# Kernel optimization log

Hardware: AMD Instinct MI355X
Metric: run time of the kernel (lower is better)

## Reference

```python
import jax, jax.numpy as jnp
import numpy as np

L_LAYERS, D, H, V, S, B = 12, 1024, 16, 50257, 512, 4
DH = D // H
DFF = 4 * D
EPS = 1e-6
STD = 0.02


def setup_inputs() -> dict:
    key = jax.random.key(0)
    ks = jax.random.split(key, 16)
    n = lambda k, shp: (jax.random.normal(k, shp, dtype=jnp.float32) * STD)
    inp = {
        'in_idx': jax.random.randint(ks[0], (B, S), 0, V, dtype=jnp.int32),
        'tok_emb': n(ks[1], (V, D)),          # tied with out_head
        'pos_emb': n(ks[2], (S, D)),
        # per-layer stacked params; Linear stored as [in, out] so y = x @ W
        'Wq': n(ks[3], (L_LAYERS, D, D)),
        'Wk': n(ks[4], (L_LAYERS, D, D)),
        'Wv': n(ks[5], (L_LAYERS, D, D)),
        'Wo': n(ks[6], (L_LAYERS, D, D)),
        'bo': jnp.zeros((L_LAYERS, D), jnp.float32),
        'W1': n(ks[7], (L_LAYERS, D, DFF)),
        'b1': jnp.zeros((L_LAYERS, DFF), jnp.float32),
        'W2': n(ks[8], (L_LAYERS, DFF, D)),
        'b2': jnp.zeros((L_LAYERS, D), jnp.float32),
        'ln1_s': jnp.ones((L_LAYERS, D), jnp.float32),
        'ln1_b': jnp.zeros((L_LAYERS, D), jnp.float32),
        'ln2_s': jnp.ones((L_LAYERS, D), jnp.float32),
        'ln2_b': jnp.zeros((L_LAYERS, D), jnp.float32),
        'lnf_s': jnp.ones((D,), jnp.float32),
        'lnf_b': jnp.zeros((D,), jnp.float32),
    }
    return inp


def _layernorm(x, scale, shift):
    mean = jnp.mean(x, axis=-1, keepdims=True)
    var = jnp.mean(jnp.square(x - mean), axis=-1, keepdims=True)  # unbiased=False
    return scale * (x - mean) / jnp.sqrt(var + EPS) + shift


def _gelu(x):
    c = jnp.sqrt(jnp.asarray(2.0 / jnp.pi, x.dtype))
    return 0.5 * x * (1.0 + jnp.tanh(c * (x + 0.044715 * x * x * x)))


def _gpt_forward(in_idx, tok_emb, pos_emb, Wq, Wk, Wv, Wo, bo, W1, b1, W2, b2,
                 ln1_s, ln1_b, ln2_s, ln2_b, lnf_s, lnf_b):
    b, s = in_idx.shape
    x = tok_emb[in_idx] + pos_emb[:s]  # [B,S,D]
    causal = jnp.triu(jnp.ones((s, s), bool), k=1)  # True above diagonal
    scale = 1.0 / jnp.sqrt(jnp.asarray(DH, x.dtype))
    for i in range(L_LAYERS):
        # --- attention sublayer ---
        h = _layernorm(x, ln1_s[i], ln1_b[i])
        q = (h @ Wq[i]).reshape(b, s, H, DH)
        k = (h @ Wk[i]).reshape(b, s, H, DH)
        v = (h @ Wv[i]).reshape(b, s, H, DH)
        scores = jnp.einsum('bqhd,bkhd->bhqk', q, k)
        scores = jnp.where(causal, -jnp.inf, scores) * scale
        attn = jax.nn.softmax(scores, axis=-1)
        ctx = jnp.einsum('bhqk,bkhd->bqhd', attn, v).reshape(b, s, D)
        x = x + ctx @ Wo[i] + bo[i]
        # --- feed-forward sublayer ---
        h = _layernorm(x, ln2_s[i], ln2_b[i])
        x = x + _gelu(h @ W1[i] + b1[i]) @ W2[i] + b2[i]
    x = _layernorm(x, lnf_s, lnf_b)
    logits = x @ tok_emb.T  # tied out head (no bias)
    return logits


def reference(in_idx, tok_emb, pos_emb, Wq, Wk, Wv, Wo, bo, W1, b1, W2, b2,
              ln1_s, ln1_b, ln2_s, ln2_b, lnf_s, lnf_b):
    return _gpt_forward(in_idx, tok_emb, pos_emb, Wq, Wk, Wv, Wo, bo, W1, b1,
                        W2, b2, ln1_s, ln1_b, ln2_s, ln2_b, lnf_s, lnf_b)
```

## Files before the change

### kernel.cpp

```cpp
#include <hip/hip_runtime.h>


#define LL 12
#define DM 1024
#define NH 16
#define DHD 64
#define NV 50257
#define NVP 50432
#define SQ 512
#define NB 4
#define DF 4096
#define MR (NB * SQ)

typedef short bf16x8 __attribute__((ext_vector_type(8)));
typedef float f32x4 __attribute__((ext_vector_type(4)));
typedef unsigned short u16;

__device__ __forceinline__ u16 f2b(float f) {
  unsigned u = __float_as_uint(f);
  u += 0x7fff + ((u >> 16) & 1);
  return (u16)(u >> 16);
}

__device__ __forceinline__ void gload16(const u16* g, u16* l) {
  __builtin_amdgcn_global_load_lds(
      (const __attribute__((address_space(1))) unsigned*)g,
      (__attribute__((address_space(3))) unsigned*)l, 16, 0, 0);
}

template <int MODE, int TBM, int TBN, int MTLOG>
__global__ __launch_bounds__(256, 2) void gemm_k(
    const u16* __restrict__ A, const u16* __restrict__ B, void* __restrict__ Cp,
    void* __restrict__ Cp2, void* __restrict__ Cp3,
    const float* __restrict__ bias, int N, int K, int lda, int ldb, int ldc) {
  int id = blockIdx.x;
  int q8 = gridDim.x >> 3;
  int swz = (id & 7) * q8 + (id >> 3);
  int mt = swz & ((1 << MTLOG) - 1), nt = swz >> MTLOG;
  int m0 = mt * TBM, n0 = nt * TBN;

  __shared__ u16 As[2][TBM * 64];
  __shared__ u16 Bs[2][TBN * 64];

  int t = threadIdx.x, lane = t & 63, wave = t >> 6;
  int wm = wave >> 1, wn = wave & 1;
  int lr = lane & 15, g = lane >> 4;
  int srow = lane >> 3;
  int sxcol = ((lane & 7) ^ (lane >> 3)) << 3;
  int rsw = (lr & 7) << 3;
  constexpr int FM = TBM / 32, FN = TBN / 32;
  constexpr int CA = TBM / 32, CB = TBN / 32;

  f32x4 acc[FM][FN];
#pragma unroll
  for (int i = 0; i < FM; ++i)
#pragma unroll
    for (int j = 0; j < FN; ++j) acc[i][j] = (f32x4){0.f, 0.f, 0.f, 0.f};

  auto stage = [&](int buf, int kt) {
    int k0 = kt * 64;
#pragma unroll
    for (int v = 0; v < CA; ++v) {
      int c = v * 4 + wave;
      gload16(A + (size_t)(m0 + c * 8 + srow) * lda + k0 + sxcol,
              &As[buf][c * 512]);
    }
#pragma unroll
    for (int v = 0; v < CB; ++v) {
      int c = v * 4 + wave;
      gload16(B + (size_t)(n0 + c * 8 + srow) * ldb + k0 + sxcol,
              &Bs[buf][c * 512]);
    }
  };

  auto compute = [&](int buf) {
    bf16x8 af[FM][2], bq[FN][2];
#pragma unroll
    for (int ks = 0; ks < 2; ++ks) {
      int co = (ks * 32 + g * 8) ^ rsw;
#pragma unroll
      for (int i = 0; i < FM; ++i)
        af[i][ks] =
            *(const bf16x8*)&As[buf][(wm * (TBM / 2) + i * 16 + lr) * 64 + co];
#pragma unroll
      for (int j = 0; j < FN; ++j)
        bq[j][ks] =
            *(const bf16x8*)&Bs[buf][(wn * (TBN / 2) + j * 16 + lr) * 64 + co];
    }
#pragma unroll
    for (int ks = 0; ks < 2; ++ks)
#pragma unroll
      for (int i = 0; i < FM; ++i)
#pragma unroll
        for (int j = 0; j < FN; ++j)
          acc[i][j] = __builtin_amdgcn_mfma_f32_16x16x32_bf16(
              af[i][ks], bq[j][ks], acc[i][j], 0, 0, 0);
  };

  int nk = K >> 6;
  stage(0, 0);
  __syncthreads();
  int cur = 0;
  for (int kt = 0; kt < nk - 1; ++kt) {
    stage(cur ^ 1, kt + 1);
    compute(cur);
    __syncthreads();
    cur ^= 1;
  }
  compute(cur);

  int rb = g * 4;
#pragma unroll
  for (int i = 0; i < FM; ++i) {
#pragma unroll
    for (int j = 0; j < FN; ++j) {
      int m = m0 + wm * (TBM / 2) + i * 16 + rb;
      int n = n0 + wn * (TBN / 2) + j * 16 + lr;
      f32x4 a = acc[i][j];
      if constexpr (MODE == 1) {
        float* C = (float*)Cp;
        float bv = bias[n];
#pragma unroll
        for (int r = 0; r < 4; ++r) {
          size_t ix = (size_t)(m + r) * ldc + n;
          C[ix] += a[r] + bv;
        }
      } else if constexpr (MODE == 2) {
        u16* C = (u16*)Cp;
        float bv = bias[n];
#pragma unroll
        for (int r = 0; r < 4; ++r) {
          float u2 = a[r] + bv;
          float gl =
              0.5f * u2 *
              (1.f + tanhf(0.7978845608f * (u2 + 0.044715f * u2 * u2 * u2)));
          C[(size_t)(m + r) * ldc + n] = f2b(gl);
        }
      } else if constexpr (MODE == 7) {
        int sel = n >> 10, nn = n & 1023;
        if (sel < 2) {
          u16* C = sel == 0 ? (u16*)Cp : (u16*)Cp2;
#pragma unroll
          for (int r = 0; r < 4; ++r) C[(size_t)(m + r) * ldc + nn] = f2b(a[r]);
        } else {
          u16* C = (u16*)Cp3;
          int bb = m >> 9, s2 = m & (SQ - 1);
          ushort4 w4;
          w4.x = f2b(a[0]); w4.y = f2b(a[1]);
          w4.z = f2b(a[2]); w4.w = f2b(a[3]);
          *(ushort4*)&C[((size_t)bb * DM + nn) * SQ + s2] = w4;
        }
      }
    }
  }
}

__global__ __launch_bounds__(512, 1) void gemmL_k(const u16* __restrict__ A,
                                                  const u16* __restrict__ B,
                                                  float* __restrict__ C) {
  int id = blockIdx.x;
  int q8 = gridDim.x >> 3;
  int swz = (id & 7) * q8 + (id >> 3);
  int mt = swz & 7, nt = swz >> 3;
  int m0 = mt * 256, n0 = nt * 256;

  __shared__ u16 As[2][256 * 64];
  __shared__ u16 Bs[3][256 * 64];

  int t = threadIdx.x, lane = t & 63, wave = t >> 6;
  int wm = wave >> 2, wn = wave & 3;
  int lr = lane & 15, g = lane >> 4;
  int rsw = (lr & 7) << 3;

  f32x4 acc[8][4];
#pragma unroll
  for (int i = 0; i < 8; ++i)
#pragma unroll
    for (int j = 0; j < 4; ++j) acc[i][j] = (f32x4){0.f, 0.f, 0.f, 0.f};

  auto stageA = [&](int slot, int kt) {
    int k0 = kt * 64;
#pragma unroll
    for (int v = 0; v < 4; ++v) {
      int c = v * 512 + t;
      int row = c >> 3, cc = c & 7;
      gload16(A + (size_t)(m0 + row) * DM + k0 + ((cc ^ (row & 7)) << 3),
              &As[slot][c * 8]);
    }
  };
  auto stageB = [&](int slot, int kt) {
    int k0 = kt * 64;
#pragma unroll
    for (int v = 0; v < 4; ++v) {
      int c = v * 512 + t;
      int row = c >> 3, cc = c & 7;
      gload16(B + (size_t)(n0 + row) * DM + k0 + ((cc ^ (row & 7)) << 3),
              &Bs[slot][c * 8]);
    }
  };
  auto compute = [&](int sa, int sb) {
#pragma unroll
    for (int ks = 0; ks < 2; ++ks) {
      int co = (ks * 32 + g * 8) ^ rsw;
      bf16x8 af[8], bq[4];
#pragma unroll
      for (int i = 0; i < 8; ++i)
        af[i] = *(const bf16x8*)&As[sa][(wm * 128 + i * 16 + lr) * 64 + co];
#pragma unroll
      for (int j = 0; j < 4; ++j)
        bq[j] = *(const bf16x8*)&Bs[sb][(wn * 64 + j * 16 + lr) * 64 + co];
      __builtin_amdgcn_s_setprio(1);
#pragma unroll
      for (int i = 0; i < 8; ++i)
#pragma unroll
        for (int j = 0; j < 4; ++j)
          acc[i][j] = __builtin_amdgcn_mfma_f32_16x16x32_bf16(
              af[i], bq[j], acc[i][j], 0, 0, 0);
      __builtin_amdgcn_s_setprio(0);
    }
  };

  stageB(0, 0); stageA(0, 0); stageB(1, 1); stageA(1, 1); stageB(2, 2);
  int sb = 0;
#pragma unroll 1
  for (int kt = 0; kt < 14; ++kt) {
    asm volatile("s_waitcnt vmcnt(12)" ::: "memory");
    __builtin_amdgcn_s_barrier();
    __builtin_amdgcn_sched_barrier(0);
    compute(kt & 1, sb);
    __builtin_amdgcn_s_barrier();
    __builtin_amdgcn_sched_barrier(0);
    stageA(kt & 1, kt + 2);
    if (kt < 13) stageB(sb, kt + 3);
    sb = sb + 1 == 3 ? 0 : sb + 1;
  }
  asm volatile("s_waitcnt vmcnt(8)" ::: "memory");
  __builtin_amdgcn_s_barrier();
  __builtin_amdgcn_sched_barrier(0);
  compute(0, 2);
  __builtin_amdgcn_s_barrier();
  __builtin_amdgcn_sched_barrier(0);
  asm volatile("s_waitcnt vmcnt(0)" ::: "memory");
  __builtin_amdgcn_s_barrier();
  __builtin_amdgcn_sched_barrier(0);
  compute(1, 0);

  int rb = g * 4;
#pragma unroll
  for (int i = 0; i < 8; ++i) {
#pragma unroll
    for (int j = 0; j < 4; ++j) {
      int m = m0 + wm * 128 + i * 16 + rb;
      int n = n0 + wn * 64 + j * 16 + lr;
      if (n < NV) {
        f32x4 a = acc[i][j];
#pragma unroll
        for (int r = 0; r < 4; ++r) C[(size_t)(m + r) * NV + n] = a[r];
      }
    }
  }
}

__global__ __launch_bounds__(256) void fattn_k(const u16* __restrict__ qb,
                                               const u16* __restrict__ kb,
                                               const u16* __restrict__ vt,
                                               u16* __restrict__ cx) {
  int id = blockIdx.x;
  int qt = id >> 6, bh = id & 63;
  int b = bh >> 4, hh = bh & 15;
  int t = threadIdx.x, lane = t & 63, w = t >> 6;
  int lr = lane & 15, g = lane >> 4;

  __shared__ u16 Kt[64 * 72];
  __shared__ u16 Vt[64 * 72];
  __shared__ u16 Pl[4 * 16 * 72];

  int qw = qt * 64 + w * 16;

  bf16x8 aQ[2];
#pragma unroll
  for (int f = 0; f < 2; ++f)
    aQ[f] = *(const bf16x8*)&qb[(size_t)(b * SQ + qw + lr) * DM + hh * DHD +
                                f * 32 + g * 8];

  f32x4 o[4];
#pragma unroll
  for (int j = 0; j < 4; ++j) o[j] = (f32x4){0.f, 0.f, 0.f, 0.f};
  f32x4 m4 = (f32x4){-3e38f, -3e38f, -3e38f, -3e38f};
  f32x4 l4 = (f32x4){0.f, 0.f, 0.f, 0.f};
  u16* Pw = &Pl[w * 16 * 72];

  for (int kt = 0; kt <= qt; ++kt) {
    int k0 = kt * 64;
#pragma unroll
    for (int it = 0; it < 2; ++it) {
      int c = t + it * 256;
      int row = c >> 3, ch = c & 7;
      int4 kv = *(const int4*)&kb[(size_t)(b * SQ + k0 + row) * DM + hh * DHD +
                                  ch * 8];
      int4 vv = *(const int4*)&vt[(size_t)(b * DM + hh * DHD + row) * SQ + k0 +
                                  ch * 8];
      *(int4*)&Kt[row * 72 + ch * 8] = kv;
      *(int4*)&Vt[row * 72 + ch * 8] = vv;
    }
    __syncthreads();

    f32x4 s[4];
#pragma unroll
    for (int j = 0; j < 4; ++j) s[j] = (f32x4){0.f, 0.f, 0.f, 0.f};
#pragma unroll
    for (int j = 0; j < 4; ++j)
#pragma unroll
      for (int f = 0; f < 2; ++f) {
        bf16x8 bk = *(const bf16x8*)&Kt[(j * 16 + lr) * 72 + f * 32 + g * 8];
        s[j] =
            __builtin_amdgcn_mfma_f32_16x16x32_bf16(aQ[f], bk, s[j], 0, 0, 0);
      }
#pragma unroll
    for (int j = 0; j < 4; ++j) {
      int kcol = k0 + j * 16 + lr;
#pragma unroll
      for (int r = 0; r < 4; ++r) {
        float sv = s[j][r] * 0.125f;
        if (kt == qt && kcol > qw + g * 4 + r) sv = -1e30f;
        s[j][r] = sv;
      }
    }
    f32x4 fr;
#pragma unroll
    for (int r = 0; r < 4; ++r) {
      float v = fmaxf(fmaxf(s[0][r], s[1][r]), fmaxf(s[2][r], s[3][r]));
#pragma unroll
      for (int d = 1; d < 16; d <<= 1) v = fmaxf(v, __shfl_xor(v, d));
      float mn = fmaxf(m4[r], v);
      fr[r] = __expf(m4[r] - mn);
      m4[r] = mn;
    }
#pragma unroll
    for (int j = 0; j < 4; ++j)
#pragma unroll
      for (int r = 0; r < 4; ++r) o[j][r] *= fr[r];
    f32x4 ps = (f32x4){0.f, 0.f, 0.f, 0.f};
#pragma unroll
    for (int j = 0; j < 4; ++j)
#pragma unroll
      for (int r = 0; r < 4; ++r) {
        float p = __expf(s[j][r] - m4[r]);
        s[j][r] = p;
        ps[r] += p;
      }
#pragma unroll
    for (int r = 0; r < 4; ++r) {
      float v = ps[r];
#pragma unroll
      for (int d = 1; d < 16; d <<= 1) v += __shfl_xor(v, d);
      l4[r] = l4[r] * fr[r] + v;
    }
#pragma unroll
    for (int j = 0; j < 4; ++j)
#pragma unroll
      for (int r = 0; r < 4; ++r)
        Pw[(g * 4 + r) * 72 + j * 16 + lr] = f2b(s[j][r]);
#pragma unroll
    for (int f = 0; f < 2; ++f) {
      bf16x8 ap = *(const bf16x8*)&Pw[lr * 72 + f * 32 + g * 8];
#pragma unroll
      for (int j = 0; j < 4; ++j) {
        bf16x8 bv = *(const bf16x8*)&Vt[(j * 16 + lr) * 72 + f * 32 + g * 8];
        o[j] = __builtin_amdgcn_mfma_f32_16x16x32_bf16(ap, bv, o[j], 0, 0, 0);
      }
    }
    __syncthreads();
  }

#pragma unroll
  for (int r = 0; r < 4; ++r) {
    float inv = 1.f / l4[r];
#pragma unroll
    for (int j = 0; j < 4; ++j)
      cx[(size_t)(b * SQ + qw + g * 4 + r) * DM + hh * DHD + j * 16 + lr] =
          f2b(o[j][r] * inv);
  }
}

__global__ __launch_bounds__(256) void transpln_k(
    const float* __restrict__ Wq, const float* __restrict__ Wk,
    const float* __restrict__ Wv, const float* __restrict__ Wo,
    const float* __restrict__ W1, const float* __restrict__ W2,
    u16* __restrict__ wb, const float* __restrict__ x,
    const float* __restrict__ sc, const float* __restrict__ sh,
    u16* __restrict__ o) {
  __shared__ u16 tl[64][72];
  __shared__ float red[8];
  int t = threadIdx.x;
  if (blockIdx.x < 3072) {
    int id = blockIdx.x;
    const float* src;
    u16* dst;
    int K, N, ktile, ntile;
    if (id < 1024) {
      int mat = id >> 8, rem = id & 255;
      ntile = rem & 15; ktile = rem >> 4;
      src = mat == 0 ? Wq : mat == 1 ? Wk : mat == 2 ? Wv : Wo;
      dst = wb + (size_t)mat * DM * DM;
      K = DM; N = DM;
    } else if (id < 2048) {
      int rem = id - 1024;
      ntile = rem & 63; ktile = rem >> 6;
      src = W1; dst = wb + (size_t)4 * DM * DM;
      K = DM; N = DF;
    } else {
      int rem = id - 2048;
      ntile = rem & 15; ktile = rem >> 4;
      src = W2; dst = wb + (size_t)4 * DM * DM + (size_t)DM * DF;
      K = DF; N = DM;
    }
    int n0 = ntile * 64, k0 = ktile * 64;
    int tn = (t & 15) * 4, tk = t >> 4;
#pragma unroll
    for (int it = 0; it < 4; ++it) {
      int k = tk + it * 16;
      float4 v = *(const float4*)(src + (size_t)(k0 + k) * N + n0 + tn);
      tl[tn + 0][k] = f2b(v.x);
      tl[tn + 1][k] = f2b(v.y);
      tl[tn + 2][k] = f2b(v.z);
      tl[tn + 3][k] = f2b(v.w);
    }
    __syncthreads();
    int wn = t >> 3, wk = (t & 7) * 8;
#pragma unroll
    for (int it = 0; it < 2; ++it) {
      int n = wn + it * 32;
      int4 v = *(const int4*)&tl[n][wk];
      *(int4*)(dst + (size_t)(n0 + n) * K + k0 + wk) = v;
    }
  } else {
    int row = blockIdx.x - 3072;
    const float* xr = x + (size_t)row * DM;
    float4 v = *(const float4*)(xr + t * 4);
    float s = v.x + v.y + v.z + v.w;
#pragma unroll
    for (int d = 32; d; d >>= 1) s += __shfl_xor(s, d);
    if ((t & 63) == 0) red[t >> 6] = s;
    __syncthreads();
    float mean = (red[0] + red[1] + red[2] + red[3]) * (1.f / DM);
    float dx = v.x - mean, dy = v.y - mean, dz = v.z - mean, dw = v.w - mean;
    float s2 = dx * dx + dy * dy + dz * dz + dw * dw;
#pragma unroll
    for (int d = 32; d; d >>= 1) s2 += __shfl_xor(s2, d);
    if ((t & 63) == 0) red[4 + (t >> 6)] = s2;
    __syncthreads();
    float var = (red[4] + red[5] + red[6] + red[7]) * (1.f / DM);
    float rstd = 1.f / sqrtf(var + 1e-6f);
    float4 gg = *(const float4*)(sc + t * 4);
    float4 b = *(const float4*)(sh + t * 4);
    ushort4 w4;
    w4.x = f2b(gg.x * (dx * rstd) + b.x);
    w4.y = f2b(gg.y * (dy * rstd) + b.y);
    w4.z = f2b(gg.z * (dz * rstd) + b.z);
    w4.w = f2b(gg.w * (dw * rstd) + b.w);
    *(ushort4*)(o + (size_t)row * DM + t * 4) = w4;
  }
}

__global__ __launch_bounds__(256) void ln_k(const float* __restrict__ x,
                                            const float* __restrict__ sc,
                                            const float* __restrict__ sh,
                                            u16* __restrict__ o) {
  int row = blockIdx.x, t = threadIdx.x;
  const float* xr = x + (size_t)row * DM;
  float4 v = *(const float4*)(xr + t * 4);
  float s = v.x + v.y + v.z + v.w;
#pragma unroll
  for (int d = 32; d; d >>= 1) s += __shfl_xor(s, d);
  __shared__ float red[8];
  if ((t & 63) == 0) red[t >> 6] = s;
  __syncthreads();
  float mean = (red[0] + red[1] + red[2] + red[3]) * (1.f / DM);
  float dx = v.x - mean, dy = v.y - mean, dz = v.z - mean, dw = v.w - mean;
  float s2 = dx * dx + dy * dy + dz * dz + dw * dw;
#pragma unroll
  for (int d = 32; d; d >>= 1) s2 += __shfl_xor(s2, d);
  if ((t & 63) == 0) red[4 + (t >> 6)] = s2;
  __syncthreads();
  float var = (red[4] + red[5] + red[6] + red[7]) * (1.f / DM);
  float rstd = 1.f / sqrtf(var + 1e-6f);
  float4 g = *(const float4*)(sc + t * 4);
  float4 b = *(const float4*)(sh + t * 4);
  ushort4 w4;
  w4.x = f2b(g.x * (dx * rstd) + b.x);
  w4.y = f2b(g.y * (dy * rstd) + b.y);
  w4.z = f2b(g.z * (dz * rstd) + b.z);
  w4.w = f2b(g.w * (dw * rstd) + b.w);
  *(ushort4*)(o + (size_t)row * DM + t * 4) = w4;
}

__global__ __launch_bounds__(256) void embtok_k(const int* __restrict__ idx,
                                                const float* __restrict__ tok,
                                                const float* __restrict__ pos,
                                                float* __restrict__ x,
                                                u16* __restrict__ tokT) {
  int t = threadIdx.x;
  if (blockIdx.x < MR) {
    int row = blockIdx.x;
    int s = row & (SQ - 1);
    int id = idx[row];
    float4 a = *(const float4*)(tok + (size_t)id * DM + t * 4);
    float4 p = *(const float4*)(pos + (size_t)s * DM + t * 4);
    a.x += p.x; a.y += p.y; a.z += p.z; a.w += p.w;
    *(float4*)(x + (size_t)row * DM + t * 4) = a;
  } else {
    size_t r = blockIdx.x - MR;
    ushort4 w = {0, 0, 0, 0};
    if (r < NV) {
      float4 v = *(const float4*)(tok + r * DM + t * 4);
      w.x = f2b(v.x); w.y = f2b(v.y); w.z = f2b(v.z); w.w = f2b(v.w);
    }
    *(ushort4*)(tokT + r * DM + t * 4) = w;
  }
}

extern "C" void kernel_launch(void* const* d_in, const int* in_sizes, int n_in,
                              void* d_out, int out_size, void* d_ws,
                              size_t ws_size, hipStream_t stream) {
  const int* idx = (const int*)d_in[0];
  const float* tok = (const float*)d_in[1];
  const float* pos = (const float*)d_in[2];
  const float* Wq = (const float*)d_in[3];
  const float* Wk = (const float*)d_in[4];
  const float* Wv = (const float*)d_in[5];
  const float* Wo = (const float*)d_in[6];
  const float* bo = (const float*)d_in[7];
  const float* W1 = (const float*)d_in[8];
  const float* b1 = (const float*)d_in[9];
  const float* W2 = (const float*)d_in[10];
  const float* b2 = (const float*)d_in[11];
  const float* ln1s = (const float*)d_in[12];
  const float* ln1b = (const float*)d_in[13];
  const float* ln2s = (const float*)d_in[14];
  const float* ln2b = (const float*)d_in[15];
  const float* lnfs = (const float*)d_in[16];
  const float* lnfb = (const float*)d_in[17];
  float* out = (float*)d_out;

  char* w = (char*)d_ws;
  float* x = (float*)w;  w += (size_t)MR * DM * 4;
  u16* h = (u16*)w;      w += (size_t)MR * DM * 2;
  u16* qb = (u16*)w;     w += (size_t)MR * DM * 2;
  u16* kb = (u16*)w;     w += (size_t)MR * DM * 2;
  u16* vt = (u16*)w;     w += (size_t)NB * DM * SQ * 2;
  u16* ff = (u16*)w;     w += (size_t)MR * DF * 2;
  u16* wb = (u16*)w;     w += ((size_t)4 * DM * DM + 2 * (size_t)DM * DF) * 2;
  u16* tokT = (u16*)w;
  u16* cx = h;
  u16* wo_b = wb + (size_t)3 * DM * DM;
  u16* wb1 = wb + (size_t)4 * DM * DM;
  u16* wb2 = wb1 + (size_t)DM * DF;

  dim3 T(256);
  embtok_k<<<MR + NVP, T, 0, stream>>>(idx, tok, pos, x, tokT);
  for (int l = 0; l < LL; ++l) {
    size_t wo_ = (size_t)l * DM * DM;
    size_t w1_ = (size_t)l * DM * DF;
    transpln_k<<<5120, T, 0, stream>>>(Wq + wo_, Wk + wo_, Wv + wo_, Wo + wo_,
                                       W1 + w1_, W2 + w1_, wb, x, ln1s + l * DM,
                                       ln1b + l * DM, h);
    gemm_k<7, 64, 128, 5><<<768, T, 0, stream>>>(
        h, wb, qb, kb, vt, nullptr, 3 * DM, DM, DM, DM, DM);
    fattn_k<<<512, T, 0, stream>>>(qb, kb, vt, cx);
    gemm_k<1, 64, 64, 5><<<512, T, 0, stream>>>(
        cx, wo_b, x, nullptr, nullptr, bo + l * DM, DM, DM, DM, DM, DM);
    ln_k<<<MR, T, 0, stream>>>(x, ln2s + l * DM, ln2b + l * DM, h);
    gemm_k<2, 128, 128, 4><<<512, T, 0, stream>>>(
        h, wb1, ff, nullptr, nullptr, b1 + l * DF, DF, DM, DM, DM, DF);
    gemm_k<1, 64, 64, 5><<<512, T, 0, stream>>>(
        ff, wb2, x, nullptr, nullptr, b2 + l * DM, DM, DF, DF, DF, DM);
  }
  ln_k<<<MR, T, 0, stream>>>(x, lnfs, lnfb, h);
  gemmL_k<<<1576, dim3(512), 0, stream>>>(h, tokT, out);
}
```

Measured before the change: 2.248 ms.

## Fuse weight fp32-to-bf16 transpose into GEMM B-tile loading

Removes the per-layer transpose/convert kernel and instead has each GEMM load fp32 weights directly from global memory into registers, convert to bf16, and write them transposed into a padded LDS tile. The QKV GEMM selects among Wq/Wk/Wv by column block. This avoids writing and re-reading the bf16 weight copy each layer, but every GEMM block now reads fp32 weights (twice the bytes) redundantly across M tiles and does conversion work plus non-async LDS scatter stores with a padded stride.

```diff
diff --git a/kernel.cpp b/kernel.cpp
--- a/kernel.cpp
+++ b/kernel.cpp
@@ -28,10 +28,13 @@
       (__attribute__((address_space(3))) unsigned*)l, 16, 0, 0);
 }
 
+#define BPAD 70
+
 template <int MODE, int TBM, int TBN, int MTLOG>
 __global__ __launch_bounds__(256, 2) void gemm_k(
-    const u16* __restrict__ A, const u16* __restrict__ B, void* __restrict__ Cp,
-    void* __restrict__ Cp2, void* __restrict__ Cp3,
+    const u16* __restrict__ A, const void* __restrict__ Bp,
+    const void* __restrict__ Bp2, const void* __restrict__ Bp3,
+    void* __restrict__ Cp, void* __restrict__ Cp2, void* __restrict__ Cp3,
     const float* __restrict__ bias, int N, int K, int lda, int ldb, int ldc) {
   int id = blockIdx.x;
   int q8 = gridDim.x >> 3;
@@ -39,8 +42,19 @@
   int mt = swz & ((1 << MTLOG) - 1), nt = swz >> MTLOG;
   int m0 = mt * TBM, n0 = nt * TBN;
 
+  const float* Bf;
+  int bn0 = n0;
+  if constexpr (MODE == 7) {
+    int sel0 = n0 >> 10;
+    Bf = sel0 == 0 ? (const float*)Bp
+                   : sel0 == 1 ? (const float*)Bp2 : (const float*)Bp3;
+    bn0 = n0 & 1023;
+  } else {
+    Bf = (const float*)Bp;
+  }
+
   __shared__ u16 As[2][TBM * 64];
-  __shared__ u16 Bs[2][TBN * 64];
+  __shared__ u16 Bs[2][TBN * BPAD];
 
   int t = threadIdx.x, lane = t & 63, wave = t >> 6;
   int wm = wave >> 1, wn = wave & 1;
@@ -49,7 +63,10 @@
   int sxcol = ((lane & 7) ^ (lane >> 3)) << 3;
   int rsw = (lr & 7) << 3;
   constexpr int FM = TBM / 32, FN = TBN / 32;
-  constexpr int CA = TBM / 32, CB = TBN / 32;
+  constexpr int CA = TBM / 32;
+
+  constexpr int LN_ = TBN / 4, KS = 256 / LN_, BP = TBN / 16;
+  int tk = t / LN_, tn = (t % LN_) * 4;
 
   f32x4 acc[FM][FN];
 #pragma unroll
@@ -57,7 +74,25 @@
 #pragma unroll
     for (int j = 0; j < FN; ++j) acc[i][j] = (f32x4){0.f, 0.f, 0.f, 0.f};
 
-  auto stage = [&](int buf, int kt) {
+  float4 breg[BP];
+  auto loadB = [&](int kt) {
+    int k0 = kt * 64;
+#pragma unroll
+    for (int p = 0; p < BP; ++p)
+      breg[p] =
+          *(const float4*)(Bf + (size_t)(k0 + p * KS + tk) * ldb + bn0 + tn);
+  };
+  auto writeB = [&](int buf) {
+#pragma unroll
+    for (int p = 0; p < BP; ++p) {
+      u16* d = &Bs[buf][tn * BPAD + p * KS + tk];
+      d[0] = f2b(breg[p].x);
+      d[BPAD] = f2b(breg[p].y);
+      d[2 * BPAD] = f2b(breg[p].z);
+      d[3 * BPAD] = f2b(breg[p].w);
+    }
+  };
+  auto stageA = [&](int buf, int kt) {
     int k0 = kt * 64;
 #pragma unroll
     for (int v = 0; v < CA; ++v) {
@@ -65,27 +100,21 @@
       gload16(A + (size_t)(m0 + c * 8 + srow) * lda + k0 + sxcol,
               &As[buf][c * 512]);
     }
-#pragma unroll
-    for (int v = 0; v < CB; ++v) {
-      int c = v * 4 + wave;
-      gload16(B + (size_t)(n0 + c * 8 + srow) * ldb + k0 + sxcol,
-              &Bs[buf][c * 512]);
-    }
-  };
-
+  };
   auto compute = [&](int buf) {
     bf16x8 af[FM][2], bq[FN][2];
 #pragma unroll
     for (int ks = 0; ks < 2; ++ks) {
       int co = (ks * 32 + g * 8) ^ rsw;
+      int cb = ks * 32 + g * 8;
 #pragma unroll
       for (int i = 0; i < FM; ++i)
         af[i][ks] =
             *(const bf16x8*)&As[buf][(wm * (TBM / 2) + i * 16 + lr) * 64 + co];
 #pragma unroll
       for (int j = 0; j < FN; ++j)
-        bq[j][ks] =
-            *(const bf16x8*)&Bs[buf][(wn * (TBN / 2) + j * 16 + lr) * 64 + co];
+        bq[j][ks] = *(const bf16x8*)&Bs[buf][(wn * (TBN / 2) + j * 16 + lr) *
+                                                 BPAD + cb];
     }
 #pragma unroll
     for (int ks = 0; ks < 2; ++ks)
@@ -98,12 +127,16 @@
   };
 
   int nk = K >> 6;
-  stage(0, 0);
+  loadB(0);
+  stageA(0, 0);
+  writeB(0);
   __syncthreads();
   int cur = 0;
   for (int kt = 0; kt < nk - 1; ++kt) {
-    stage(cur ^ 1, kt + 1);
+    loadB(kt + 1);
+    stageA(cur ^ 1, kt + 1);
     compute(cur);
+    writeB(cur ^ 1);
     __syncthreads();
     cur ^= 1;
   }
@@ -380,86 +413,6 @@
     for (int j = 0; j < 4; ++j)
       cx[(size_t)(b * SQ + qw + g * 4 + r) * DM + hh * DHD + j * 16 + lr] =
           f2b(o[j][r] * inv);
-  }
-}
-
-__global__ __launch_bounds__(256) void transpln_k(
-    const float* __restrict__ Wq, const float* __restrict__ Wk,
-    const float* __restrict__ Wv, const float* __restrict__ Wo,
-    const float* __restrict__ W1, const float* __restrict__ W2,
-    u16* __restrict__ wb, const float* __restrict__ x,
-    const float* __restrict__ sc, const float* __restrict__ sh,
-    u16* __restrict__ o) {
-  __shared__ u16 tl[64][72];
-  __shared__ float red[8];
-  int t = threadIdx.x;
-  if (blockIdx.x < 3072) {
-    int id = blockIdx.x;
-    const float* src;
-    u16* dst;
-    int K, N, ktile, ntile;
-    if (id < 1024) {
-      int mat = id >> 8, rem = id & 255;
-      ntile = rem & 15; ktile = rem >> 4;
-      src = mat == 0 ? Wq : mat == 1 ? Wk : mat == 2 ? Wv : Wo;
-      dst = wb + (size_t)mat * DM * DM;
-      K = DM; N = DM;
-    } else if (id < 2048) {
-      int rem = id - 1024;
-      ntile = rem & 63; ktile = rem >> 6;
-      src = W1; dst = wb + (size_t)4 * DM * DM;
-      K = DM; N = DF;
-    } else {
-      int rem = id - 2048;
-      ntile = rem & 15; ktile = rem >> 4;
-      src = W2; dst = wb + (size_t)4 * DM * DM + (size_t)DM * DF;
-      K = DF; N = DM;
-    }
-    int n0 = ntile * 64, k0 = ktile * 64;
-    int tn = (t & 15) * 4, tk = t >> 4;
-#pragma unroll
-    for (int it = 0; it < 4; ++it) {
-      int k = tk + it * 16;
-      float4 v = *(const float4*)(src + (size_t)(k0 + k) * N + n0 + tn);
-      tl[tn + 0][k] = f2b(v.x);
-      tl[tn + 1][k] = f2b(v.y);
-      tl[tn + 2][k] = f2b(v.z);
-      tl[tn + 3][k] = f2b(v.w);
-    }
-    __syncthreads();
-    int wn = t >> 3, wk = (t & 7) * 8;
-#pragma unroll
-    for (int it = 0; it < 2; ++it) {
-      int n = wn + it * 32;
-      int4 v = *(const int4*)&tl[n][wk];
-      *(int4*)(dst + (size_t)(n0 + n) * K + k0 + wk) = v;
-    }
-  } else {
-    int row = blockIdx.x - 3072;
-    const float* xr = x + (size_t)row * DM;
-    float4 v = *(const float4*)(xr + t * 4);
-    float s = v.x + v.y + v.z + v.w;
-#pragma unroll
-    for (int d = 32; d; d >>= 1) s += __shfl_xor(s, d);
-    if ((t & 63) == 0) red[t >> 6] = s;
-    __syncthreads();
-    float mean = (red[0] + red[1] + red[2] + red[3]) * (1.f / DM);
-    float dx = v.x - mean, dy = v.y - mean, dz = v.z - mean, dw = v.w - mean;
-    float s2 = dx * dx + dy * dy + dz * dz + dw * dw;
-#pragma unroll
-    for (int d = 32; d; d >>= 1) s2 += __shfl_xor(s2, d);
-    if ((t & 63) == 0) red[4 + (t >> 6)] = s2;
-    __syncthreads();
-    float var = (red[4] + red[5] + red[6] + red[7]) * (1.f / DM);
-    float rstd = 1.f / sqrtf(var + 1e-6f);
-    float4 gg = *(const float4*)(sc + t * 4);
-    float4 b = *(const float4*)(sh + t * 4);
-    ushort4 w4;
-    w4.x = f2b(gg.x * (dx * rstd) + b.x);
-    w4.y = f2b(gg.y * (dy * rstd) + b.y);
-    w4.z = f2b(gg.z * (dz * rstd) + b.z);
-    w4.w = f2b(gg.w * (dw * rstd) + b.w);
-    *(ushort4*)(o + (size_t)row * DM + t * 4) = w4;
   }
 }
 
@@ -550,31 +503,29 @@
   u16* kb = (u16*)w;     w += (size_t)MR * DM * 2;
   u16* vt = (u16*)w;     w += (size_t)NB * DM * SQ * 2;
   u16* ff = (u16*)w;     w += (size_t)MR * DF * 2;
-  u16* wb = (u16*)w;     w += ((size_t)4 * DM * DM + 2 * (size_t)DM * DF) * 2;
   u16* tokT = (u16*)w;
   u16* cx = h;
-  u16* wo_b = wb + (size_t)3 * DM * DM;
-  u16* wb1 = wb + (size_t)4 * DM * DM;
-  u16* wb2 = wb1 + (size_t)DM * DF;
 
   dim3 T(256);
   embtok_k<<<MR + NVP, T, 0, stream>>>(idx, tok, pos, x, tokT);
   for (int l = 0; l < LL; ++l) {
     size_t wo_ = (size_t)l * DM * DM;
     size_t w1_ = (size_t)l * DM * DF;
-    transpln_k<<<5120, T, 0, stream>>>(Wq + wo_, Wk + wo_, Wv + wo_, Wo + wo_,
-                                       W1 + w1_, W2 + w1_, wb, x, ln1s + l * DM,
-                                       ln1b + l * DM, h);
+    ln_k<<<MR, T, 0, stream>>>(x, ln1s + l * DM, ln1b + l * DM, h);
     gemm_k<7, 64, 128, 5><<<768, T, 0, stream>>>(
-        h, wb, qb, kb, vt, nullptr, 3 * DM, DM, DM, DM, DM);
+        h, Wq + wo_, Wk + wo_, Wv + wo_, qb, kb, vt, nullptr, 3 * DM, DM, DM,
+        DM, DM);
     fattn_k<<<512, T, 0, stream>>>(qb, kb, vt, cx);
     gemm_k<1, 64, 64, 5><<<512, T, 0, stream>>>(
-        cx, wo_b, x, nullptr, nullptr, bo + l * DM, DM, DM, DM, DM, DM);
+        cx, Wo + wo_, nullptr, nullptr, x, nullptr, nullptr, bo + l * DM, DM,
+        DM, DM, DM, DM);
     ln_k<<<MR, T, 0, stream>>>(x, ln2s + l * DM, ln2b + l * DM, h);
     gemm_k<2, 128, 128, 4><<<512, T, 0, stream>>>(
-        h, wb1, ff, nullptr, nullptr, b1 + l * DF, DF, DM, DM, DM, DF);
+        h, W1 + w1_, nullptr, nullptr, ff, nullptr, nullptr, b1 + l * DF, DF,
+        DM, DM, DF, DF);
     gemm_k<1, 64, 64, 5><<<512, T, 0, stream>>>(
-        ff, wb2, x, nullptr, nullptr, b2 + l * DM, DM, DF, DF, DF, DM);
+        ff, W2 + w1_, nullptr, nullptr, x, nullptr, nullptr, b2 + l * DM, DM,
+        DF, DF, DM, DM);
   }
   ln_k<<<MR, T, 0, stream>>>(x, lnfs, lnfb, h);
   gemmL_k<<<1576, dim3(512), 0, stream>>>(h, tokT, out);
```

Result: slower. 3.134 ms (+39.4%).
